# Kernel optimization log

Measured on AMD Instinct MI355X. Metric: run time of the kernel, lower is better.

## Reference

```python
import jax, jax.numpy as jnp
import numpy as np

B, P, K = 32, 1024, 20  # clouds, points per cloud, kNN neighbors
EPS = 1e-5


def knn_idx(x, k):
    # x: [B,P,d] -> indices of k nearest neighbors (squared L2, includes self), [B,P,k]
    d2 = jnp.sum(x * x, axis=-1)
    dist = d2[:, :, None] + d2[:, None, :] - 2.0 * jnp.einsum('bpd,bqd->bpq', x, x)
    _, idx = jax.lax.top_k(-dist, k)
    return idx


def edge_conv(x, idx, msg_fn):
    # gather neighbor features, build [x_i, x_j - x_i] edge features, max-aggregate
    xj = jax.vmap(lambda xb, ib: xb[ib])(x, idx)            # [B,P,K,d]
    xi = jnp.broadcast_to(x[:, :, None, :], xj.shape)       # [B,P,K,d]
    e = jnp.concatenate([xi, xj - xi], axis=-1)             # [B,P,K,2d]
    return jnp.max(msg_fn(e), axis=2)                       # [B,P,out]


def setup_inputs() -> dict:
    key = jax.random.key(0)
    ks = jax.random.split(key, 5)
    s = 0.05
    return {
        'pos': jax.random.normal(ks[0], (B * P, 3), jnp.float32),
        'W1a': jax.random.normal(ks[1], (6, 64), jnp.float32) * s,
        'b1a': jnp.zeros((64,), jnp.float32),
        'g1': jnp.ones((64,), jnp.float32),
        'be1': jnp.zeros((64,), jnp.float32),
        'W1b': jax.random.normal(ks[2], (64, 64), jnp.float32) * s,
        'b1b': jnp.zeros((64,), jnp.float32),
        'W2': jax.random.normal(ks[3], (128, 128), jnp.float32) * s,
        'b2': jnp.zeros((128,), jnp.float32),
        'Wl': jax.random.normal(ks[4], (192, 128), jnp.float32) * s,
        'bl': jnp.zeros((128,), jnp.float32),
        'batch': jnp.repeat(jnp.arange(B, dtype=jnp.int32), P),
    }


def reference(pos, W1a, b1a, g1, be1, W1b, b1b, W2, b2, Wl, bl, batch):
    # batch is uniform-sized and sorted -> fixed reshape to [B,P,.]
    x0 = pos.reshape(B, P, 3)

    def mlp1(e):  # Linear(6,64) -> BatchNorm -> ReLU -> Linear(64,64)
        h = e @ W1a + b1a
        mu = jnp.mean(h, axis=(0, 1, 2))
        var = jnp.var(h, axis=(0, 1, 2))
        h = (h - mu) * jax.lax.rsqrt(var + EPS) * g1 + be1
        h = jax.nn.relu(h)
        return h @ W1b + b1b

    x1 = edge_conv(x0, knn_idx(x0, K), mlp1)                         # [B,P,64]
    x2 = edge_conv(x1, knn_idx(x1, K), lambda e: e @ W2 + b2)        # [B,P,128]
    h = jnp.concatenate([x1, x2], axis=-1) @ Wl + bl                 # [B,P,128]
    return jnp.max(h, axis=1)                                        # global_max_pool -> [B,128]
```

## Files before the change

### kernel.cpp

```cpp
#include <hip/hip_runtime.h>
#include <cfloat>
#include <cstdint>

#define NB 32
#define NP 1024
#define NK 20
#define NPTS 32768

typedef __attribute__((ext_vector_type(8))) short bf16x8;
typedef __attribute__((ext_vector_type(4))) float f32x4;

__device__ __forceinline__ unsigned bf16rne(float v) {
  const unsigned u = __float_as_uint(v);
  return (u + 0x7fffu + ((u >> 16) & 1u)) >> 16;
}

__device__ __forceinline__ float unsort_f(unsigned s) {
  const unsigned m = (~(unsigned)((int)s >> 31)) | 0x80000000u;
  return __uint_as_float(s ^ m);
}

__global__ __launch_bounds__(256) void kd2(const float* __restrict__ x, int dim,
                                           float* __restrict__ d2) {
  int p = blockIdx.x * 256 + threadIdx.x;
  if (p >= NPTS) return;
  if (dim == 64) {
    const float4* xr = (const float4*)(x + (size_t)p * 64);
    float s = 0.f;
#pragma unroll
    for (int dq = 0; dq < 16; dq++) {
      float4 v = xr[dq];
      s = fmaf(v.x, v.x, s);
      s = fmaf(v.y, v.y, s);
      s = fmaf(v.z, v.z, s);
      s = fmaf(v.w, v.w, s);
    }
    d2[p] = s;
  } else {
    float s = 0.f;
#pragma unroll
    for (int d = 0; d < 3; d++) {
      float v = x[p * 3 + d];
      s = fmaf(v, v, s);
    }
    d2[p] = s;
  }
}

__global__ __launch_bounds__(256) void kxprep(const float* __restrict__ x,
                                              unsigned short* __restrict__ Xh,
                                              unsigned short* __restrict__ Xl) {
  const int t = blockIdx.x * 256 + threadIdx.x;
  const int p = t >> 3, g = t & 7;
  const float4* xr = (const float4*)(x + (size_t)p * 64 + g * 8);
  const float4 v0 = xr[0];
  const float4 v1 = xr[1];
  const float vv[8] = {v0.x, v0.y, v0.z, v0.w, v1.x, v1.y, v1.z, v1.w};
  unsigned short h[8], l[8];
#pragma unroll
  for (int j = 0; j < 8; j++) {
    const float z = vv[j];
    const unsigned u = __float_as_uint(z);
    const unsigned hb = (u + 0x7fffu + ((u >> 16) & 1u)) & 0xffff0000u;
    h[j] = (unsigned short)(hb >> 16);
    l[j] = (unsigned short)bf16rne(z - __uint_as_float(hb));
  }
  const int off = (((p >> 4) * 2 + (g >> 2)) * 64 + ((g & 3) << 4) + (p & 15)) * 8;
  *(uint4*)&Xh[off] = *(const uint4*)&h[0];
  *(uint4*)&Xl[off] = *(const uint4*)&l[0];
}

__global__ __launch_bounds__(256) void kdistm(const unsigned short* __restrict__ Xh,
                                              const unsigned short* __restrict__ Xl,
                                              const float* __restrict__ d2,
                                              int c0, int nc, float* __restrict__ D) {
  const int lane = threadIdx.x & 63;
  const int w = threadIdx.x >> 6;
  const int cloud = blockIdx.x % nc;
  const int t = blockIdx.x / nc;
  const int tr0 = (t >> 3) * 128, tc0 = (t & 7) * 128;
  const int cb = (c0 + cloud) * 1024;
  const int rw = tr0 + w * 32;

  bf16x8 Ah[2][2], Al[2][2];
#pragma unroll
  for (int mt = 0; mt < 2; mt++)
#pragma unroll
    for (int ks = 0; ks < 2; ks++) {
      const int tg = (cb + rw + mt * 16) >> 4;
      const size_t base = ((size_t)(tg * 2 + ks) * 64 + lane) * 8;
      Ah[mt][ks] = *(const bf16x8*)&Xh[base];
      Al[mt][ks] = *(const bf16x8*)&Xl[base];
    }
  float d2r[2][4];
#pragma unroll
  for (int mt = 0; mt < 2; mt++)
#pragma unroll
    for (int r = 0; r < 4; r++)
      d2r[mt][r] = d2[cb + rw + mt * 16 + (lane >> 4) * 4 + r];

  for (int nt = 0; nt < 8; nt++) {
    const int cg = cb + tc0 + nt * 16;
    bf16x8 Bh2[2], Bl2[2];
#pragma unroll
    for (int ks = 0; ks < 2; ks++) {
      const int tg = cg >> 4;
      const size_t base = ((size_t)(tg * 2 + ks) * 64 + lane) * 8;
      Bh2[ks] = *(const bf16x8*)&Xh[base];
      Bl2[ks] = *(const bf16x8*)&Xl[base];
    }
    const float d2c = d2[cg + (lane & 15)];
#pragma unroll
    for (int mt = 0; mt < 2; mt++) {
      f32x4 C = {0.f, 0.f, 0.f, 0.f};
      C = __builtin_amdgcn_mfma_f32_16x16x32_bf16(Ah[mt][0], Bh2[0], C, 0, 0, 0);
      C = __builtin_amdgcn_mfma_f32_16x16x32_bf16(Ah[mt][0], Bl2[0], C, 0, 0, 0);
      C = __builtin_amdgcn_mfma_f32_16x16x32_bf16(Al[mt][0], Bh2[0], C, 0, 0, 0);
      C = __builtin_amdgcn_mfma_f32_16x16x32_bf16(Ah[mt][1], Bh2[1], C, 0, 0, 0);
      C = __builtin_amdgcn_mfma_f32_16x16x32_bf16(Ah[mt][1], Bl2[1], C, 0, 0, 0);
      C = __builtin_amdgcn_mfma_f32_16x16x32_bf16(Al[mt][1], Bh2[1], C, 0, 0, 0);
#pragma unroll
      for (int r = 0; r < 4; r++) {
        const int row = cloud * 1024 + rw + mt * 16 + (lane >> 4) * 4 + r;
        const int col = tc0 + nt * 16 + (lane & 15);
        D[(size_t)row * 1024 + col] = fmaf(-2.f, C[r], d2r[mt][r] + d2c);
      }
    }
  }
}

__device__ __forceinline__ void select20(const float* dv, unsigned long long* w,
                                         int lane, int pg, int gbase,
                                         int* __restrict__ idxo) {
  unsigned k32[16];
#pragma unroll
  for (int ii = 0; ii < 16; ii++) {
    unsigned u = __float_as_uint(dv[ii]);
    u ^= (((int)u >> 31) | 0x80000000u);
    k32[ii] = u;
  }
  unsigned lmn = k32[0];
#pragma unroll
  for (int ii = 1; ii < 16; ii++) lmn = k32[ii] < lmn ? k32[ii] : lmn;
  unsigned mn = lmn, mlm = lmn;
#pragma unroll
  for (int s = 1; s < 64; s <<= 1) {
    const unsigned a = __shfl_xor(mn, s, 64);
    const unsigned b = __shfl_xor(mlm, s, 64);
    mn = a < mn ? a : mn;
    mlm = b > mlm ? b : mlm;
  }
  unsigned lo32 = mn;
  unsigned long long hi32 = (unsigned long long)mlm + 1;
  float flo = unsort_f(mn), fhi = unsort_f(mlm);
  float clo = 0.f, chi = 140.f;
  unsigned m32 = 0;
  bool found = false;
  for (int it = 0; it < 40; ++it) {
    if (hi32 - (unsigned long long)lo32 <= 1) break;
    unsigned m;
    if (it < 6) {
      float fr = (42.f - clo) / (chi - clo);
      fr = fr < 0.04f ? 0.04f : (fr > 0.96f ? 0.96f : fr);
      const float pf = fmaf(fhi - flo, fr, flo);
      unsigned u = __float_as_uint(pf);
      u ^= (((int)u >> 31) | 0x80000000u);
      m = u;
      if (m <= lo32) m = lo32 + 1;
      if ((unsigned long long)m >= hi32) m = (unsigned)(hi32 - 1);
    } else {
      m = (unsigned)(lo32 + ((hi32 - lo32) >> 1));
    }
    int cnt = 0;
#pragma unroll
    for (int ii = 0; ii < 16; ii++) cnt += __popcll(__ballot(k32[ii] < m));
    if (cnt < 20) {
      lo32 = m;
      flo = unsort_f(m);
      clo = (float)cnt;
    } else if (cnt > 64) {
      hi32 = m;
      fhi = unsort_f(m);
      chi = (float)cnt;
    } else {
      m32 = m;
      found = true;
      break;
    }
  }

  if (found) {
    unsigned mask = 0;
#pragma unroll
    for (int ii = 0; ii < 16; ii++) mask |= (k32[ii] < m32) ? (1u << ii) : 0u;
    const int lc = __popc(mask);
    int x = lc;
#pragma unroll
    for (int s = 1; s < 64; s <<= 1) {
      const int y = __shfl_up(x, s, 64);
      if (lane >= s) x += y;
    }
    int off = x - lc;
    w[lane] = ~0ULL;
    __builtin_amdgcn_wave_barrier();
#pragma unroll
    for (int i = 0; i < 4; i++)
#pragma unroll
      for (int j = 0; j < 4; j++) {
        const int ii = i * 4 + j;
        if ((mask & (1u << ii)) && off < 64) {
          w[off] = ((unsigned long long)k32[ii] << 10) |
                   (unsigned)(i * 256 + (lane << 2) + j);
          off++;
        }
      }
    __builtin_amdgcn_wave_barrier();
    unsigned long long K = w[lane];
#pragma unroll
    for (int k = 2; k <= 64; k <<= 1) {
#pragma unroll
      for (int j2 = k >> 1; j2 > 0; j2 >>= 1) {
        const unsigned long long o = __shfl_xor(K, j2, 64);
        const bool takeMin = (((lane & j2) == 0) == ((lane & k) == 0));
        const bool lt = K < o;
        const unsigned long long sml = lt ? K : o;
        const unsigned long long big = lt ? o : K;
        K = takeMin ? sml : big;
      }
    }
    if (lane < NK) idxo[(size_t)pg * NK + lane] = gbase + (int)(K & 1023u);
  } else {
    unsigned long long lo64 = ((unsigned long long)lo32) << 10;
    unsigned long long hi64 = hi32 << 10;
    unsigned long long cut = hi64;
    for (int it = 0; it < 48 && (hi64 - lo64) > 1; ++it) {
      const unsigned long long m = lo64 + ((hi64 - lo64) >> 1);
      int cnt = 0;
#pragma unroll
      for (int ii = 0; ii < 16; ii++) {
        const unsigned long long key =
            ((unsigned long long)k32[ii] << 10) |
            (unsigned)(((ii >> 2) << 8) + (lane << 2) + (ii & 3));
        cnt += __popcll(__ballot(key < m));
      }
      if (cnt == 20) {
        cut = m;
        break;
      }
      if (cnt < 20)
        lo64 = m;
      else
        hi64 = m;
      cut = hi64;
    }
    int base = 0;
#pragma unroll
    for (int ii = 0; ii < 16; ii++) {
      const unsigned long long key =
          ((unsigned long long)k32[ii] << 10) |
          (unsigned)(((ii >> 2) << 8) + (lane << 2) + (ii & 3));
      const unsigned long long b = __ballot(key < cut);
      if (key < cut) {
        const int slot = base + __builtin_amdgcn_mbcnt_hi(
                                    (unsigned)(b >> 32),
                                    __builtin_amdgcn_mbcnt_lo((unsigned)b, 0));
        idxo[(size_t)pg * NK + slot] = gbase + (int)(key & 1023u);
      }
      base += __popcll(b);
    }
  }
}

__global__ __launch_bounds__(512) void kfsel1(const float* __restrict__ pos,
                                              const float* __restrict__ d2,
                                              int* __restrict__ idxo) {
  __shared__ float px[1024], py[1024], pz[1024], pd2[1024];
  __shared__ unsigned long long lw[8][64];
  const int tid = threadIdx.x;
  const int lane = tid & 63;
  const int w = tid >> 6;
  const int cloud = blockIdx.x >> 7;
  const int mb = blockIdx.x & 127;
  const int cb = cloud << 10;

  if (tid < 256) {
    const float4* ppos = (const float4*)(pos + (size_t)cb * 3 + tid * 12);
    const float4 a = ppos[0], b = ppos[1], c = ppos[2];
    *(float4*)&px[tid * 4] = make_float4(a.x, a.w, b.z, c.y);
    *(float4*)&py[tid * 4] = make_float4(a.y, b.x, b.w, c.z);
    *(float4*)&pz[tid * 4] = make_float4(a.z, b.y, c.x, c.w);
  }
  *(float2*)&pd2[tid * 2] = *(const float2*)(d2 + cb + tid * 2);
  __syncthreads();

  const int pl = mb * 8 + w;
  const float xi0 = px[pl], xi1 = py[pl], xi2 = pz[pl];
  const float dp = pd2[pl];
  float dv[16];
#pragma unroll
  for (int i = 0; i < 4; i++) {
    const float4 X = *(const float4*)&px[i * 256 + lane * 4];
    const float4 Y = *(const float4*)&py[i * 256 + lane * 4];
    const float4 Z = *(const float4*)&pz[i * 256 + lane * 4];
    const float4 Q = *(const float4*)&pd2[i * 256 + lane * 4];
    const float xs[4] = {X.x, X.y, X.z, X.w};
    const float ys[4] = {Y.x, Y.y, Y.z, Y.w};
    const float zs[4] = {Z.x, Z.y, Z.z, Z.w};
    const float qs[4] = {Q.x, Q.y, Q.z, Q.w};
#pragma unroll
    for (int j = 0; j < 4; j++) {
      float acc = 0.f;
      acc = fmaf(xi0, xs[j], acc);
      acc = fmaf(xi1, ys[j], acc);
      acc = fmaf(xi2, zs[j], acc);
      dv[i * 4 + j] = fmaf(-2.f, acc, dp + qs[j]);
    }
  }
  select20(dv, lw[w], lane, cb + pl, cb, idxo);
}

__global__ __launch_bounds__(256) void kselect2(const float* __restrict__ D,
                                                int c0, int* __restrict__ idxo) {
  __shared__ unsigned long long lw[4][64];
  const int lane = threadIdx.x & 63;
  const int sub = threadIdx.x >> 6;
  const int pchunk = blockIdx.x * 4 + sub;
  const int pg = c0 * 1024 + pchunk;
  const int gbase = (pg >> 10) << 10;

  float dv[16];
  const float4* dr = (const float4*)(D + (size_t)pchunk * 1024 + lane * 4);
#pragma unroll
  for (int i = 0; i < 4; i++) {
    const float4 d4 = dr[i * 64];
    dv[i * 4 + 0] = d4.x;
    dv[i * 4 + 1] = d4.y;
    dv[i * 4 + 2] = d4.z;
    dv[i * 4 + 3] = d4.w;
  }
  select20(dv, lw[sub], lane, pg, gbase, idxo);
}

__global__ __launch_bounds__(256) void kstats(const float* __restrict__ pos,
                                              const int* __restrict__ idx,
                                              double* __restrict__ Spart) {
  __shared__ float red[4][42];
  const int tid = threadIdx.x;
  const int w = tid >> 6;
  int p = blockIdx.x * 256 + tid;
  float xi0 = pos[p * 3], xi1 = pos[p * 3 + 1], xi2 = pos[p * 3 + 2];
  float s1[6];
  float s2[36];
#pragma unroll
  for (int a = 0; a < 6; a++) s1[a] = 0.f;
#pragma unroll
  for (int a = 0; a < 36; a++) s2[a] = 0.f;
  for (int k = 0; k < NK; k++) {
    int j = idx[p * NK + k];
    float e[6];
    e[0] = xi0;
    e[1] = xi1;
    e[2] = xi2;
    e[3] = pos[j * 3] - xi0;
    e[4] = pos[j * 3 + 1] - xi1;
    e[5] = pos[j * 3 + 2] - xi2;
#pragma unroll
    for (int a = 0; a < 6; a++) {
      s1[a] += e[a];
#pragma unroll
      for (int b = 0; b < 6; b++) s2[a * 6 + b] = fmaf(e[a], e[b], s2[a * 6 + b]);
    }
  }
#pragma unroll
  for (int a = 0; a < 6; a++) {
#pragma unroll
    for (int m = 1; m < 64; m <<= 1) s1[a] += __shfl_xor(s1[a], m, 64);
  }
#pragma unroll
  for (int a = 0; a < 36; a++) {
#pragma unroll
    for (int m = 1; m < 64; m <<= 1) s2[a] += __shfl_xor(s2[a], m, 64);
  }
  if ((tid & 63) == 0) {
#pragma unroll
    for (int a = 0; a < 6; a++) red[w][a] = s1[a];
#pragma unroll
    for (int a = 0; a < 36; a++) red[w][6 + a] = s2[a];
  }
  __syncthreads();
  if (tid < 42) {
    double t = (double)red[0][tid] + (double)red[1][tid] + (double)red[2][tid] +
               (double)red[3][tid];
    Spart[(size_t)blockIdx.x * 42 + tid] = t;
  }
}

__global__ void kbn(const double* __restrict__ Spart, const float* __restrict__ W1a,
                    const float* __restrict__ b1a, const float* __restrict__ g1,
                    const float* __restrict__ be1, const float* __restrict__ W1b,
                    float* __restrict__ ss, unsigned short* __restrict__ Bh,
                    unsigned short* __restrict__ Bl) {
  __shared__ double S[42];
  const int c = threadIdx.x;
  if (c < 42) {
    double t = 0.0;
    for (int b = 0; b < 128; b++) t += Spart[(size_t)b * 42 + c];
    S[c] = t;
  }
  for (int t = c; t < 4096; t += 256) {
    const int j = t & 7, L = (t >> 3) & 63, f = t >> 9;
    const int nt = f >> 1, ks = f & 1;
    const int k = ks * 32 + (L >> 4) * 8 + j;
    const int n = nt * 16 + (L & 15);
    const float wv = W1b[k * 64 + n];
    const unsigned u = __float_as_uint(wv);
    const unsigned hb = (u + 0x7fffu + ((u >> 16) & 1u)) & 0xffff0000u;
    Bh[t] = (unsigned short)(hb >> 16);
    Bl[t] = (unsigned short)bf16rne(wv - __uint_as_float(hb));
  }
  __syncthreads();
  if (c < 64) {
    double w[6];
#pragma unroll
    for (int d = 0; d < 6; d++) w[d] = (double)W1a[d * 64 + c];
    double b = (double)b1a[c];
    const double invN = 1.0 / (double)((size_t)NPTS * NK);
    double m1 = 0.0;
#pragma unroll
    for (int d = 0; d < 6; d++) m1 += w[d] * S[d];
    m1 *= invN;
    double q = 0.0;
#pragma unroll
    for (int a = 0; a < 6; a++)
#pragma unroll
      for (int d = 0; d < 6; d++) q += w[a] * w[d] * S[6 + a * 6 + d];
    q *= invN;
    double mu = m1 + b;
    double eh2 = q + 2.0 * b * m1 + b * b;
    double var = eh2 - mu * mu;
    if (var < 0.0) var = 0.0;
    double inv = 1.0 / sqrt(var + 1e-5);
    double sc = (double)g1[c] * inv;
    ss[c] = (float)sc;
    ss[64 + c] = (float)((double)be1[c] - mu * sc);
  }
}

#define EC1P 8
__global__ __launch_bounds__(256) void kec1(const float* __restrict__ pos,
                                            const int* __restrict__ idx,
                                            const float* __restrict__ ss,
                                            const float* __restrict__ W1a,
                                            const float* __restrict__ b1a,
                                            const unsigned short* __restrict__ Bh,
                                            const unsigned short* __restrict__ Bl,
                                            const float* __restrict__ b1b,
                                            float* __restrict__ x1) {
  __shared__ __align__(16) unsigned short Ah[4][3072];
  __shared__ __align__(16) unsigned short Al[4][3072];
  __shared__ float nbr[4][160];
  const int tid = threadIdx.x;
  const int lane = tid & 63;
  const int w = tid >> 6;
  const int p0 = blockIdx.x * EC1P + w * 2;

  unsigned short* ah = Ah[w];
  unsigned short* al = Al[w];
  float* nb = nbr[w];

  if (lane < 40) {
    const int j = idx[(size_t)p0 * NK + lane];
    nb[lane * 4 + 0] = pos[j * 3 + 0];
    nb[lane * 4 + 1] = pos[j * 3 + 1];
    nb[lane * 4 + 2] = pos[j * 3 + 2];
  }

  float wdf[3], wbt[3];
#pragma unroll
  for (int d = 0; d < 3; d++) {
    const float top = W1a[d * 64 + lane];
    const float bot = W1a[(3 + d) * 64 + lane];
    wdf[d] = top - bot;
    wbt[d] = bot;
  }
  const float b1 = b1a[lane];
  const float sc = ss[lane];
  const float sh = ss[64 + lane];
  const int lanepart = ((lane >> 5) * 512) + (((lane & 31) >> 3) * 128) + (lane & 7);
  __builtin_amdgcn_wave_barrier();

#pragma unroll
  for (int pp = 0; pp < 2; pp++) {
    const int p = p0 + pp;
    const float xi0 = pos[p * 3], xi1 = pos[p * 3 + 1], xi2 = pos[p * 3 + 2];
    const float pu = fmaf(xi2, wdf[2], fmaf(xi1, wdf[1], fmaf(xi0, wdf[0], b1)));
    for (int k = 0; k < NK; k++) {
      const int row = pp * NK + k;
      const float4 nbv = *(const float4*)&nb[row * 4];
      const float pv = fmaf(nbv.z, wbt[2], fmaf(nbv.y, wbt[1], nbv.x * wbt[0]));
      const float z = fmaxf(fmaf(pu + pv, sc, sh), 0.f);
      const unsigned u = __float_as_uint(z);
      const unsigned hb = (u + 0x7fffu + ((u >> 16) & 1u)) & 0xffff0000u;
      const int off = (row >> 4) * 1024 + (row & 15) * 8 + lanepart;
      ah[off] = (unsigned short)(hb >> 16);
      al[off] = (unsigned short)bf16rne(z - __uint_as_float(hb));
    }
  }
  __builtin_amdgcn_wave_barrier();

  bf16x8 bh[4][2], bl[4][2];
#pragma unroll
  for (int nt = 0; nt < 4; nt++)
#pragma unroll
    for (int ks = 0; ks < 2; ks++) {
      const int base = ((nt * 2 + ks) * 64 + lane) * 8;
      bh[nt][ks] = *(const bf16x8*)&Bh[base];
      bl[nt][ks] = *(const bf16x8*)&Bl[base];
    }

  float pA[4], pB[4];
#pragma unroll
  for (int nt = 0; nt < 4; nt++) {
    pA[nt] = -FLT_MAX;
    pB[nt] = -FLT_MAX;
  }
  const int q4 = (lane >> 4) * 4;

#pragma unroll
  for (int mt = 0; mt < 3; mt++) {
    const bf16x8 a_h0 = *(const bf16x8*)&ah[mt * 1024 + lane * 8];
    const bf16x8 a_l0 = *(const bf16x8*)&al[mt * 1024 + lane * 8];
    const bf16x8 a_h1 = *(const bf16x8*)&ah[mt * 1024 + 512 + lane * 8];
    const bf16x8 a_l1 = *(const bf16x8*)&al[mt * 1024 + 512 + lane * 8];
#pragma unroll
    for (int nt = 0; nt < 4; nt++) {
      f32x4 C = {0.f, 0.f, 0.f, 0.f};
      C = __builtin_amdgcn_mfma_f32_16x16x32_bf16(a_h0, bh[nt][0], C, 0, 0, 0);
      C = __builtin_amdgcn_mfma_f32_16x16x32_bf16(a_h0, bl[nt][0], C, 0, 0, 0);
      C = __builtin_amdgcn_mfma_f32_16x16x32_bf16(a_l0, bh[nt][0], C, 0, 0, 0);
      C = __builtin_amdgcn_mfma_f32_16x16x32_bf16(a_h1, bh[nt][1], C, 0, 0, 0);
      C = __builtin_amdgcn_mfma_f32_16x16x32_bf16(a_h1, bl[nt][1], C, 0, 0, 0);
      C = __builtin_amdgcn_mfma_f32_16x16x32_bf16(a_l1, bh[nt][1], C, 0, 0, 0);
#pragma unroll
      for (int r = 0; r < 4; r++) {
        const int row = mt * 16 + q4 + r;
        const float vv = C[r];
        if (row < NK) pA[nt] = fmaxf(pA[nt], vv);
        if (row >= NK && row < 2 * NK) pB[nt] = fmaxf(pB[nt], vv);
      }
    }
  }
#pragma unroll
  for (int s = 16; s < 64; s <<= 1) {
#pragma unroll
    for (int nt = 0; nt < 4; nt++) {
      pA[nt] = fmaxf(pA[nt], __shfl_xor(pA[nt], s, 64));
      pB[nt] = fmaxf(pB[nt], __shfl_xor(pB[nt], s, 64));
    }
  }
  if (lane < 16) {
#pragma unroll
    for (int nt = 0; nt < 4; nt++) {
      const float bb = b1b[nt * 16 + lane];
      x1[(size_t)p0 * 64 + nt * 16 + lane] = pA[nt] + bb;
      x1[(size_t)(p0 + 1) * 64 + nt * 16 + lane] = pB[nt] + bb;
    }
  }
}

__global__ __launch_bounds__(256) void kv(const float* __restrict__ x1,
                                          const float* __restrict__ W2,
                                          float* __restrict__ v) {
  const int c = threadIdx.x & 127;
  const int sub = threadIdx.x >> 7;
  float wv[64];
#pragma unroll
  for (int d = 0; d < 64; d++) wv[d] = W2[(64 + d) * 128 + c];
  const int pbase = blockIdx.x * 64 + sub * 32;
  for (int i = 0; i < 32; i++) {
    const int p = pbase + i;
    const float4* xr = (const float4*)(x1 + (size_t)p * 64);
    float a0 = 0.f, a1 = 0.f;
#pragma unroll
    for (int dq = 0; dq < 16; dq++) {
      float4 xv = xr[dq];
      a0 = fmaf(xv.x, wv[dq * 4 + 0], a0);
      a1 = fmaf(xv.y, wv[dq * 4 + 1], a1);
      a0 = fmaf(xv.z, wv[dq * 4 + 2], a0);
      a1 = fmaf(xv.w, wv[dq * 4 + 3], a1);
    }
    v[(size_t)p * 128 + c] = a0 + a1;
  }
}

__global__ __launch_bounds__(256) void kprep(const float* __restrict__ W2,
                                             const float* __restrict__ Wl,
                                             const float* __restrict__ b2,
                                             const float* __restrict__ bl,
                                             float* __restrict__ Bc,
                                             float* __restrict__ cb) {
  const int t = blockIdx.x * 256 + threadIdx.x;
  const int d = t >> 7, c = t & 127;
  float s = Wl[d * 128 + c];
  for (int e = 0; e < 128; e++)
    s = fmaf(W2[d * 128 + e] - W2[(64 + d) * 128 + e], Wl[(64 + e) * 128 + c], s);
  Bc[d * 128 + c] = s;
  Bc[(64 + 2 * d) * 128 + c] = Wl[(64 + 2 * d) * 128 + c];
  Bc[(64 + 2 * d + 1) * 128 + c] = Wl[(64 + 2 * d + 1) * 128 + c];
  if (d == 0) {
    float sb = bl[c];
    for (int e = 0; e < 128; e++) sb = fmaf(b2[e], Wl[(64 + e) * 128 + c], sb);
    cb[c] = sb;
  }
}

#define ATS 72
#define BSS 132
__global__ __launch_bounds__(256) void kgemm(const float* __restrict__ x1,
                                             const float* __restrict__ v,
                                             const int* __restrict__ idx,
                                             const float* __restrict__ Bc,
                                             float* __restrict__ partial) {
  __shared__ float AT[192 * ATS];
  __shared__ float BS[16 * BSS];
  int* idxs = (int*)BS;
  const int tid = threadIdx.x;
  const int cloud = blockIdx.x & 31;
  const int mb = blockIdx.x >> 5;
  const int pbase = cloud * 1024 + mb * 64;

#pragma unroll
  for (int r = 0; r < 5; r++) {
    int id = r * 256 + tid;
    idxs[id] = idx[(size_t)pbase * NK + id];
  }
#pragma unroll
  for (int r = 0; r < 16; r++) {
    int id = r * 256 + tid;
    int m = id >> 6, k = id & 63;
    AT[k * ATS + m] = x1[(size_t)(pbase + m) * 64 + k];
  }
  __syncthreads();
#pragma unroll
  for (int r = 0; r < 32; r++) {
    int id = r * 256 + tid;
    int m = id >> 7, kk = id & 127;
    const int* ip = &idxs[m * NK];
    float mx = -FLT_MAX;
#pragma unroll
    for (int k = 0; k < NK; k++) mx = fmaxf(mx, v[(size_t)ip[k] * 128 + kk]);
    AT[(64 + kk) * ATS + m] = mx;
  }
  __syncthreads();

  const int tr = tid >> 4, tc = tid & 15;
  float acc[4][8];
#pragma unroll
  for (int i = 0; i < 4; i++)
#pragma unroll
    for (int n = 0; n < 8; n++) acc[i][n] = 0.f;
  for (int kc = 0; kc < 12; kc++) {
#pragma unroll
    for (int r = 0; r < 8; r++) {
      int id = r * 256 + tid;
      int row = id >> 7, col = id & 127;
      BS[row * BSS + col] = Bc[(size_t)(kc * 16 + row) * 128 + col];
    }
    __syncthreads();
#pragma unroll
    for (int k = 0; k < 16; k++) {
      int kg = kc * 16 + k;
      float4 a = *(const float4*)&AT[kg * ATS + tr * 4];
      float4 b0 = *(const float4*)&BS[k * BSS + tc * 8];
      float4 b1 = *(const float4*)&BS[k * BSS + tc * 8 + 4];
      float av[4] = {a.x, a.y, a.z, a.w};
      float bv[8] = {b0.x, b0.y, b0.z, b0.w, b1.x, b1.y, b1.z, b1.w};
#pragma unroll
      for (int i = 0; i < 4; i++)
#pragma unroll
        for (int n = 0; n < 8; n++) acc[i][n] = fmaf(av[i], bv[n], acc[i][n]);
    }
    __syncthreads();
  }
#pragma unroll
  for (int n = 0; n < 8; n++) {
    float m4 = fmaxf(fmaxf(acc[0][n], acc[1][n]), fmaxf(acc[2][n], acc[3][n]));
    BS[tr * BSS + tc * 8 + n] = m4;
  }
  __syncthreads();
  if (tid < 128) {
    float m = -FLT_MAX;
#pragma unroll
    for (int rr = 0; rr < 16; rr++) m = fmaxf(m, BS[rr * BSS + tid]);
    partial[(size_t)(cloud * 16 + mb) * 128 + tid] = m;
  }
}

__global__ __launch_bounds__(256) void kred(const float* __restrict__ partial,
                                            const float* __restrict__ cb,
                                            float* __restrict__ out) {
  int t = blockIdx.x * 256 + threadIdx.x;
  int b = t >> 7, c = t & 127;
  float m = -FLT_MAX;
#pragma unroll
  for (int mb = 0; mb < 16; mb++) m = fmaxf(m, partial[(size_t)(b * 16 + mb) * 128 + c]);
  out[t] = m + cb[c];
}

extern "C" void kernel_launch(void* const* d_in, const int* in_sizes, int n_in,
                              void* d_out, int out_size, void* d_ws, size_t ws_size,
                              hipStream_t stream) {
  const float* pos = (const float*)d_in[0];
  const float* W1a = (const float*)d_in[1];
  const float* b1a = (const float*)d_in[2];
  const float* g1 = (const float*)d_in[3];
  const float* be1 = (const float*)d_in[4];
  const float* W1b = (const float*)d_in[5];
  const float* b1b = (const float*)d_in[6];
  const float* W2 = (const float*)d_in[7];
  const float* b2 = (const float*)d_in[8];
  const float* Wl = (const float*)d_in[9];
  const float* bl = (const float*)d_in[10];
  float* out = (float*)d_out;

  float* ws = (float*)d_ws;
  float* x1 = ws;
  float* v = ws + 2097152;
  int* idx = (int*)(ws + 6291456);
  float* d2b = ws + 6946816;
  double* Spart = (double*)(ws + 6979584);
  float* Bc = ws + 6990336;
  float* cb = ws + 7014912;
  float* ss = ws + 7015040;
  unsigned short* Bh = (unsigned short*)(ws + 7015168);
  unsigned short* Bl = (unsigned short*)(ws + 7017216);
  float* partial = ws + 7019264;
  unsigned short* Xfh = (unsigned short*)(ws + 7084800);
  unsigned short* Xfl = (unsigned short*)(ws + 8133376);
  const size_t base = 9181952;
  float* D = ws + base;

  if (ws_size < (base + 1024 * 1024) * sizeof(float)) return;

  size_t avail = ws_size / sizeof(float) - base;
  int nc = 1;
  for (int c = 32; c >= 1; c >>= 1)
    if ((size_t)c * 1024 * 1024 <= avail) {
      nc = c;
      break;
    }

  kd2<<<128, 256, 0, stream>>>(pos, 3, d2b);
  kfsel1<<<NB * 128, 512, 0, stream>>>(pos, d2b, idx);

  kstats<<<128, 256, 0, stream>>>(pos, idx, Spart);
  kbn<<<1, 256, 0, stream>>>(Spart, W1a, b1a, g1, be1, W1b, ss, Bh, Bl);
  kec1<<<NPTS / EC1P, 256, 0, stream>>>(pos, idx, ss, W1a, b1a, Bh, Bl, b1b, x1);

  kd2<<<128, 256, 0, stream>>>(x1, 64, d2b);
  kxprep<<<1024, 256, 0, stream>>>(x1, Xfh, Xfl);
  for (int c0 = 0; c0 < NB; c0 += nc) {
    kdistm<<<nc * 64, 256, 0, stream>>>(Xfh, Xfl, d2b, c0, nc, D);
    kselect2<<<nc * 256, 256, 0, stream>>>(D, c0, idx);
  }

  kv<<<512, 256, 0, stream>>>(x1, W2, v);
  kprep<<<32, 256, 0, stream>>>(W2, Wl, b2, bl, Bc, cb);
  kgemm<<<512, 256, 0, stream>>>(x1, v, idx, Bc, partial);
  kred<<<16, 256, 0, stream>>>(partial, cb, out);
}
```

Measured before the change: 340.7 us.

## Move final GEMM to bf16 split-precision MFMA with vectorized neighbor max gather

```diff
diff --git a/kernel.cpp b/kernel.cpp
--- a/kernel.cpp
+++ b/kernel.cpp
@@ -614,85 +614,137 @@
   }
 }
 
-#define ATS 72
-#define BSS 132
+__global__ __launch_bounds__(256) void kprep2(const float* __restrict__ Bc,
+                                              unsigned short* __restrict__ Bch,
+                                              unsigned short* __restrict__ Bcl) {
+  const int t = blockIdx.x * 256 + threadIdx.x;
+  const int j = t & 7, L = (t >> 3) & 63, f = t >> 9;
+  const int nt = f / 6, kc = f % 6;
+  const int k = kc * 32 + ((L >> 4) << 3) + j;
+  const int n = nt * 16 + (L & 15);
+  const float wv = Bc[k * 128 + n];
+  const unsigned u = __float_as_uint(wv);
+  const unsigned hb = (u + 0x7fffu + ((u >> 16) & 1u)) & 0xffff0000u;
+  Bch[t] = (unsigned short)(hb >> 16);
+  Bcl[t] = (unsigned short)bf16rne(wv - __uint_as_float(hb));
+}
+
 __global__ __launch_bounds__(256) void kgemm(const float* __restrict__ x1,
                                              const float* __restrict__ v,
                                              const int* __restrict__ idx,
-                                             const float* __restrict__ Bc,
+                                             const unsigned short* __restrict__ Bch,
+                                             const unsigned short* __restrict__ Bcl,
                                              float* __restrict__ partial) {
-  __shared__ float AT[192 * ATS];
-  __shared__ float BS[16 * BSS];
-  int* idxs = (int*)BS;
+  __shared__ __align__(16) unsigned short Ah[12288];
+  __shared__ __align__(16) unsigned short Al[12288];
+  __shared__ int idxs[1280];
+  __shared__ float red[4][8][16];
   const int tid = threadIdx.x;
+  const int lane = tid & 63;
+  const int w = tid >> 6;
   const int cloud = blockIdx.x & 31;
   const int mb = blockIdx.x >> 5;
   const int pbase = cloud * 1024 + mb * 64;
+  const int mrow = lane & 15, gsel = lane >> 4;
 
 #pragma unroll
   for (int r = 0; r < 5; r++) {
-    int id = r * 256 + tid;
+    const int id = r * 256 + tid;
     idxs[id] = idx[(size_t)pbase * NK + id];
   }
-#pragma unroll
-  for (int r = 0; r < 16; r++) {
-    int id = r * 256 + tid;
-    int m = id >> 6, k = id & 63;
-    AT[k * ATS + m] = x1[(size_t)(pbase + m) * 64 + k];
+
+#pragma unroll
+  for (int rr = 0; rr < 2; rr++) {
+    const int mt = w, kc = rr;
+    const int m = mt * 16 + mrow;
+    const float4* xr =
+        (const float4*)(x1 + (size_t)(pbase + m) * 64 + kc * 32 + gsel * 8);
+    const float4 v0 = xr[0], v1 = xr[1];
+    const float vv[8] = {v0.x, v0.y, v0.z, v0.w, v1.x, v1.y, v1.z, v1.w};
+    unsigned short h8[8], l8[8];
+#pragma unroll
+    for (int j = 0; j < 8; j++) {
+      const unsigned u = __float_as_uint(vv[j]);
+      const unsigned hb = (u + 0x7fffu + ((u >> 16) & 1u)) & 0xffff0000u;
+      h8[j] = (unsigned short)(hb >> 16);
+      l8[j] = (unsigned short)bf16rne(vv[j] - __uint_as_float(hb));
+    }
+    const int a16 = (mt * 6 + kc) * 64 + lane;
+    *(uint4*)&Ah[a16 * 8] = *(const uint4*)h8;
+    *(uint4*)&Al[a16 * 8] = *(const uint4*)l8;
   }
   __syncthreads();
-#pragma unroll
-  for (int r = 0; r < 32; r++) {
-    int id = r * 256 + tid;
-    int m = id >> 7, kk = id & 127;
+
+#pragma unroll
+  for (int rr = 0; rr < 4; rr++) {
+    const int i3 = rr * 4 + w;
+    const int mt = i3 & 3, kg_hi = i3 >> 2;
+    const int m = mt * 16 + mrow;
+    const int kk0 = (kg_hi * 4 + gsel) * 8;
     const int* ip = &idxs[m * NK];
-    float mx = -FLT_MAX;
-#pragma unroll
-    for (int k = 0; k < NK; k++) mx = fmaxf(mx, v[(size_t)ip[k] * 128 + kk]);
-    AT[(64 + kk) * ATS + m] = mx;
+    float mx[8];
+#pragma unroll
+    for (int j = 0; j < 8; j++) mx[j] = -FLT_MAX;
+    for (int k = 0; k < NK; k++) {
+      const float4* vr = (const float4*)(v + (size_t)ip[k] * 128 + kk0);
+      const float4 a = vr[0], b = vr[1];
+      mx[0] = fmaxf(mx[0], a.x);
+      mx[1] = fmaxf(mx[1], a.y);
+      mx[2] = fmaxf(mx[2], a.z);
+      mx[3] = fmaxf(mx[3], a.w);
+      mx[4] = fmaxf(mx[4], b.x);
+      mx[5] = fmaxf(mx[5], b.y);
+      mx[6] = fmaxf(mx[6], b.z);
+      mx[7] = fmaxf(mx[7], b.w);
+    }
+    unsigned short h8[8], l8[8];
+#pragma unroll
+    for (int j = 0; j < 8; j++) {
+      const unsigned u = __float_as_uint(mx[j]);
+      const unsigned hb = (u + 0x7fffu + ((u >> 16) & 1u)) & 0xffff0000u;
+      h8[j] = (unsigned short)(hb >> 16);
+      l8[j] = (unsigned short)bf16rne(mx[j] - __uint_as_float(hb));
+    }
+    const int a16 = (mt * 6 + 2 + kg_hi) * 64 + lane;
+    *(uint4*)&Ah[a16 * 8] = *(const uint4*)h8;
+    *(uint4*)&Al[a16 * 8] = *(const uint4*)l8;
   }
   __syncthreads();
 
-  const int tr = tid >> 4, tc = tid & 15;
-  float acc[4][8];
-#pragma unroll
-  for (int i = 0; i < 4; i++)
-#pragma unroll
-    for (int n = 0; n < 8; n++) acc[i][n] = 0.f;
-  for (int kc = 0; kc < 12; kc++) {
-#pragma unroll
-    for (int r = 0; r < 8; r++) {
-      int id = r * 256 + tid;
-      int row = id >> 7, col = id & 127;
-      BS[row * BSS + col] = Bc[(size_t)(kc * 16 + row) * 128 + col];
-    }
-    __syncthreads();
-#pragma unroll
-    for (int k = 0; k < 16; k++) {
-      int kg = kc * 16 + k;
-      float4 a = *(const float4*)&AT[kg * ATS + tr * 4];
-      float4 b0 = *(const float4*)&BS[k * BSS + tc * 8];
-      float4 b1 = *(const float4*)&BS[k * BSS + tc * 8 + 4];
-      float av[4] = {a.x, a.y, a.z, a.w};
-      float bv[8] = {b0.x, b0.y, b0.z, b0.w, b1.x, b1.y, b1.z, b1.w};
-#pragma unroll
-      for (int i = 0; i < 4; i++)
-#pragma unroll
-        for (int n = 0; n < 8; n++) acc[i][n] = fmaf(av[i], bv[n], acc[i][n]);
-    }
-    __syncthreads();
-  }
-#pragma unroll
-  for (int n = 0; n < 8; n++) {
-    float m4 = fmaxf(fmaxf(acc[0][n], acc[1][n]), fmaxf(acc[2][n], acc[3][n]));
-    BS[tr * BSS + tc * 8 + n] = m4;
+  f32x4 acc[8];
+#pragma unroll
+  for (int nt = 0; nt < 8; nt++) acc[nt] = {0.f, 0.f, 0.f, 0.f};
+  const int mt = w;
+#pragma unroll
+  for (int kc = 0; kc < 6; kc++) {
+    const int a16 = (mt * 6 + kc) * 64 + lane;
+    const bf16x8 a_h = *(const bf16x8*)&Ah[a16 * 8];
+    const bf16x8 a_l = *(const bf16x8*)&Al[a16 * 8];
+#pragma unroll
+    for (int nt = 0; nt < 8; nt++) {
+      const size_t bo = ((size_t)(nt * 6 + kc) * 64 + lane) * 8;
+      const bf16x8 b_h = *(const bf16x8*)&Bch[bo];
+      const bf16x8 b_l = *(const bf16x8*)&Bcl[bo];
+      acc[nt] = __builtin_amdgcn_mfma_f32_16x16x32_bf16(a_h, b_h, acc[nt], 0, 0, 0);
+      acc[nt] = __builtin_amdgcn_mfma_f32_16x16x32_bf16(a_h, b_l, acc[nt], 0, 0, 0);
+      acc[nt] = __builtin_amdgcn_mfma_f32_16x16x32_bf16(a_l, b_h, acc[nt], 0, 0, 0);
+      acc[nt] = __builtin_amdgcn_mfma_f32_16x16x32_bf16(a_l, b_l, acc[nt], 0, 0, 0);
+    }
+  }
+
+#pragma unroll
+  for (int nt = 0; nt < 8; nt++) {
+    float rm = fmaxf(fmaxf(acc[nt][0], acc[nt][1]), fmaxf(acc[nt][2], acc[nt][3]));
+    rm = fmaxf(rm, __shfl_xor(rm, 16, 64));
+    rm = fmaxf(rm, __shfl_xor(rm, 32, 64));
+    if (lane < 16) red[w][nt][lane] = rm;
   }
   __syncthreads();
   if (tid < 128) {
-    float m = -FLT_MAX;
-#pragma unroll
-    for (int rr = 0; rr < 16; rr++) m = fmaxf(m, BS[rr * BSS + tid]);
-    partial[(size_t)(cloud * 16 + mb) * 128 + tid] = m;
+    const int nt = tid >> 4, cc = tid & 15;
+    const float m4 = fmaxf(fmaxf(red[0][nt][cc], red[1][nt][cc]),
+                           fmaxf(red[2][nt][cc], red[3][nt][cc]));
+    partial[(size_t)(cloud * 16 + mb) * 128 + tid] = m4;
   }
 }
 
@@ -737,7 +789,9 @@
   float* partial = ws + 7019264;
   unsigned short* Xfh = (unsigned short*)(ws + 7084800);
   unsigned short* Xfl = (unsigned short*)(ws + 8133376);
-  const size_t base = 9181952;
+  unsigned short* Bch2 = (unsigned short*)(ws + 9181952);
+  unsigned short* Bcl2 = (unsigned short*)(ws + 9194240);
+  const size_t base = 9206528;
   float* D = ws + base;
 
   if (ws_size < (base + 1024 * 1024) * sizeof(float)) return;
@@ -766,6 +820,7 @@
 
   kv<<<512, 256, 0, stream>>>(x1, W2, v);
   kprep<<<32, 256, 0, stream>>>(W2, Wl, b2, bl, Bc, cb);
-  kgemm<<<512, 256, 0, stream>>>(x1, v, idx, Bc, partial);
+  kprep2<<<96, 256, 0, stream>>>(Bc, Bch2, Bcl2);
+  kgemm<<<512, 256, 0, stream>>>(x1, v, idx, Bch2, Bcl2, partial);
   kred<<<16, 256, 0, stream>>>(partial, cb, out);
 }
```

After: 354.2 us. 1.04x slower.
